# Kernel tuning notes

Measured on AMD Instinct MI355X. Metric: run time of the kernel, lower is better.

Reference implementation:

```python
import jax, jax.numpy as jnp
import numpy as np

L, H, D, E, V, MAXS = 12, 12, 64, 768, 50257, 1024

def _ln(x, g, b, eps=1e-5):
    m = jnp.mean(x, axis=-1, keepdims=True)
    v = jnp.mean(jnp.square(x - m), axis=-1, keepdims=True)
    return (x - m) * jax.lax.rsqrt(v + eps) * g + b

def setup_inputs() -> dict:
    key = jax.random.key(0)
    ks = jax.random.split(key, 16)
    s = 0.02
    inp = {
        "input_ids": jax.random.randint(ks[0], (1, 1), 0, V),
        "past_key": jax.random.normal(ks[1], (L, 1, H, MAXS, D), jnp.float32),
        "past_value": jax.random.normal(ks[2], (L, 1, H, MAXS, D), jnp.float32),
        "past_seq_len": 1023,
        "attention_mask": jnp.ones((1, MAXS), jnp.float32),
        "wte": jax.random.normal(ks[3], (V, E), jnp.float32) * s,
        "wpe": jax.random.normal(ks[4], (MAXS, E), jnp.float32) * s,
        "ln1_g": jnp.ones((L, E), jnp.float32),
        "ln1_b": jnp.zeros((L, E), jnp.float32),
        "attn_w": jax.random.normal(ks[5], (L, E, 3 * E), jnp.float32) * s,
        "attn_b": jnp.zeros((L, 3 * E), jnp.float32),
        "proj_w": jax.random.normal(ks[6], (L, E, E), jnp.float32) * s,
        "proj_b": jnp.zeros((L, E), jnp.float32),
        "ln2_g": jnp.ones((L, E), jnp.float32),
        "ln2_b": jnp.zeros((L, E), jnp.float32),
        "fc_w": jax.random.normal(ks[7], (L, E, 4 * E), jnp.float32) * s,
        "fc_b": jnp.zeros((L, 4 * E), jnp.float32),
        "mlp_w": jax.random.normal(ks[8], (L, 4 * E, E), jnp.float32) * s,
        "mlp_b": jnp.zeros((L, E), jnp.float32),
        "lnf_g": jnp.ones((E,), jnp.float32),
        "lnf_b": jnp.zeros((E,), jnp.float32),
    }
    return inp

def reference(input_ids, past_key, past_value, past_seq_len, attention_mask,
              wte, wpe, ln1_g, ln1_b, attn_w, attn_b, proj_w, proj_b,
              ln2_g, ln2_b, fc_w, fc_b, mlp_w, mlp_b, lnf_g, lnf_b):
    S = int(past_seq_len)  # static cache length
    h = wte[input_ids] + wpe[S]                      # [1,1,E]
    bias = (1.0 - attention_mask[:, :S + 1]) * -1e9  # [1,S+1]
    scale = 1.0 / jnp.sqrt(jnp.float32(D))
    pk, pv = past_key, past_value
    for l in range(L):
        x = _ln(h, ln1_g[l], ln1_b[l])
        qkv = x @ attn_w[l] + attn_b[l]              # [1,1,3E]
        q, k, v = jnp.split(qkv, 3, axis=-1)
        q = q.reshape(1, 1, H, D).transpose(0, 2, 1, 3)  # [1,H,1,D]
        k = k.reshape(1, 1, H, D).transpose(0, 2, 1, 3)
        v = v.reshape(1, 1, H, D).transpose(0, 2, 1, 3)
        k_full = jnp.concatenate([pk[l, :, :, :S, :], k], axis=2)  # [1,H,S+1,D]
        v_full = jnp.concatenate([pv[l, :, :, :S, :], v], axis=2)
        scores = jnp.einsum('bhqd,bhkd->bhqk', q, k_full) * scale
        scores = scores + bias[:, None, None, :]
        attn = jax.nn.softmax(scores, axis=-1)
        o = jnp.einsum('bhqk,bhkd->bhqd', attn, v_full)
        o = o.transpose(0, 2, 1, 3).reshape(1, 1, H * D)
        h = h + o @ proj_w[l] + proj_b[l]
        x2 = _ln(h, ln2_g[l], ln2_b[l])
        h = h + jax.nn.gelu(x2 @ fc_w[l] + fc_b[l], approximate=True) @ mlp_w[l] + mlp_b[l]
        pk = pk.at[l, :, :, S, :].set(k[:, :, 0, :])
        pv = pv.at[l, :, :, S, :].set(v[:, :, 0, :])
    h = _ln(h, lnf_g, lnf_b)
    logits = h @ wte.T                               # [1,1,V] (tied lm_head)
    return (logits, pk, pv)
```

## Files before the change

kernel.cpp:

```cpp
#include <hip/hip_runtime.h>
#include <math.h>

#define EMB 768
#define NH 12
#define HD 64
#define NL 12
#define NV 50257
#define MAXS 1024
#define S_PAST 1023
#define E3 2304
#define E4 3072

#define WS_H    0
#define WS_QKV  768
#define WS_FC   3072
#define WS_PART 6144

__device__ __forceinline__ void blockReduce2(float& a, float& b, volatile float* ra, volatile float* rb) {
  int lane = threadIdx.x & 63, wid = threadIdx.x >> 6;
#pragma unroll
  for (int o = 32; o > 0; o >>= 1) { a += __shfl_down(a, o); b += __shfl_down(b, o); }
  if (lane == 0) { ra[wid] = a; rb[wid] = b; }
  __syncthreads();
  if (threadIdx.x == 0) {
    ra[0] = ra[0] + ra[1] + ra[2] + ra[3];
    rb[0] = rb[0] + rb[1] + rb[2] + rb[3];
  }
  __syncthreads();
  a = ra[0]; b = rb[0];
}

__global__ void init_kernel(const int* __restrict__ ids, const float* __restrict__ wte,
                            const float* __restrict__ wpe, const float* __restrict__ attn_b,
                            float* __restrict__ hvec, float* __restrict__ qkv) {
  int idx = blockIdx.x * 256 + threadIdx.x;
  if (idx < E3) qkv[idx] = attn_b[idx];
  if (idx < EMB) {
    int id = ids[0];
    hvec[idx] = wte[(size_t)id * EMB + idx] + wpe[(size_t)S_PAST * EMB + idx];
  }
}

__global__ void ln_gemv4(const float* __restrict__ hvec, const float* __restrict__ g,
                         const float* __restrict__ bb, const float* __restrict__ W,
                         float* __restrict__ out, int N, int l) {
  __shared__ float lh[EMB];
  __shared__ float xs[32];
  __shared__ float ra[4], rb[4];
  __shared__ float4 red[4][64];
  int tid = threadIdx.x, lane = tid & 63, wid = tid >> 6;
  int e0 = blockIdx.y * 32;
  float hv0 = hvec[tid], hv1 = hvec[tid + 256], hv2 = hvec[tid + 512];
  int j4 = blockIdx.x * 64 + lane;
  int N4 = N >> 2;
  const float4* p = (const float4*)(W + (size_t)l * EMB * N) + (size_t)(e0 + wid) * N4 + j4;
  float4 w[8];
#pragma unroll
  for (int i = 0; i < 8; i++) w[i] = p[(size_t)(i * 4) * N4];
  float gv = 0.f, bv = 0.f;
  if (tid < 32) { gv = g[l * EMB + e0 + tid]; bv = bb[l * EMB + e0 + tid]; }
  lh[tid] = hv0; lh[tid + 256] = hv1; lh[tid + 512] = hv2;
  float s1 = hv0 + hv1 + hv2;
  float s2 = hv0 * hv0 + hv1 * hv1 + hv2 * hv2;
  blockReduce2(s1, s2, ra, rb);
  float mean = s1 * (1.f / EMB);
  float var = s2 * (1.f / EMB) - mean * mean;
  float rstd = rsqrtf(var + 1e-5f);
  if (tid < 32) xs[tid] = (lh[e0 + tid] - mean) * rstd * gv + bv;
  __syncthreads();
  float4 acc = {0.f, 0.f, 0.f, 0.f};
#pragma unroll
  for (int i = 0; i < 8; i++) {
    float x = xs[wid + i * 4];
    acc.x += x * w[i].x; acc.y += x * w[i].y; acc.z += x * w[i].z; acc.w += x * w[i].w;
  }
  red[wid][lane] = acc;
  __syncthreads();
  if (wid == 0) {
    float4 a0 = red[0][lane], a1 = red[1][lane], a2 = red[2][lane], a3 = red[3][lane];
    float rx = a0.x + a1.x + a2.x + a3.x;
    float ry = a0.y + a1.y + a2.y + a3.y;
    float rz = a0.z + a1.z + a2.z + a3.z;
    float rw = a0.w + a1.w + a2.w + a3.w;
    float* op = out + (size_t)j4 * 4;
    atomicAdd(op + 0, rx); atomicAdd(op + 1, ry);
    atomicAdd(op + 2, rz); atomicAdd(op + 3, rw);
  }
}

__global__ void attn_kv(const float* __restrict__ qkv, const float* __restrict__ pk,
                        const float* __restrict__ pv, const float* __restrict__ mask,
                        float* __restrict__ opk, float* __restrict__ opv,
                        float* __restrict__ part, int l) {
  int h = blockIdx.x >> 4, c = blockIdx.x & 15;
  int tid = threadIdx.x, lane = tid & 63, wid = tid >> 6;
  int sub = tid & 15, grp = tid >> 4;
  __shared__ float4 qs4[16];
  __shared__ float sc[64];
  __shared__ float4 redo[4][16];
  if (tid < 16) qs4[tid] = ((const float4*)(qkv + h * 64))[tid];
  __syncthreads();
  size_t base = ((size_t)(l * NH + h) * MAXS) * HD;
  const float4* K4 = (const float4*)(pk + base);
  const float4* V4 = (const float4*)(pv + base);
  float4* oK4 = (float4*)(opk + base);
  float4* oV4 = (float4*)(opv + base);
  int t0 = c * 64;
  float4 kreg[4];
#pragma unroll
  for (int i = 0; i < 4; i++) {
    int t = t0 + grp + i * 16;
    kreg[i] = (t == S_PAST) ? ((const float4*)(qkv + EMB + h * 64))[sub] : K4[(size_t)t * 16 + sub];
  }
#pragma unroll
  for (int i = 0; i < 4; i++) {
    int t = t0 + grp + i * 16;
    oK4[(size_t)t * 16 + sub] = kreg[i];
  }
  float4 q4 = qs4[sub];
#pragma unroll
  for (int i = 0; i < 4; i++) {
    int key = grp + i * 16;
    float p = q4.x * kreg[i].x + q4.y * kreg[i].y + q4.z * kreg[i].z + q4.w * kreg[i].w;
    p += __shfl_xor(p, 1); p += __shfl_xor(p, 2);
    p += __shfl_xor(p, 4); p += __shfl_xor(p, 8);
    if (sub == 0) sc[key] = p * 0.125f + (1.f - mask[t0 + key]) * (-1e9f);
  }
  __syncthreads();
  if (wid == 0) {
    float a = sc[lane];
    float m = a;
#pragma unroll
    for (int o = 32; o > 0; o >>= 1) m = fmaxf(m, __shfl_down(m, o));
    m = __shfl(m, 0);
    float ea = expf(a - m);
    sc[lane] = ea;
    float s = ea;
#pragma unroll
    for (int o = 32; o > 0; o >>= 1) s += __shfl_down(s, o);
    if (lane == 0) { part[(h * 16 + c) * 68 + 0] = m; part[(h * 16 + c) * 68 + 1] = s; }
  }
  __syncthreads();
  float4 vreg[4];
#pragma unroll
  for (int i = 0; i < 4; i++) {
    int t = t0 + grp + i * 16;
    vreg[i] = (t == S_PAST) ? ((const float4*)(qkv + 2 * EMB + h * 64))[sub] : V4[(size_t)t * 16 + sub];
  }
#pragma unroll
  for (int i = 0; i < 4; i++) {
    int t = t0 + grp + i * 16;
    oV4[(size_t)t * 16 + sub] = vreg[i];
  }
  float4 acc = {0.f, 0.f, 0.f, 0.f};
#pragma unroll
  for (int i = 0; i < 4; i++) {
    float w = sc[grp + i * 16];
    acc.x += w * vreg[i].x; acc.y += w * vreg[i].y; acc.z += w * vreg[i].z; acc.w += w * vreg[i].w;
  }
  acc.x += __shfl_xor(acc.x, 16); acc.y += __shfl_xor(acc.y, 16);
  acc.z += __shfl_xor(acc.z, 16); acc.w += __shfl_xor(acc.w, 16);
  acc.x += __shfl_xor(acc.x, 32); acc.y += __shfl_xor(acc.y, 32);
  acc.z += __shfl_xor(acc.z, 32); acc.w += __shfl_xor(acc.w, 32);
  if (lane < 16) redo[wid][lane] = acc;
  __syncthreads();
  if (tid < 16) {
    float4 a0 = redo[0][tid], a1 = redo[1][tid], a2 = redo[2][tid], a3 = redo[3][tid];
    float4 r;
    r.x = a0.x + a1.x + a2.x + a3.x;
    r.y = a0.y + a1.y + a2.y + a3.y;
    r.z = a0.z + a1.z + a2.z + a3.z;
    r.w = a0.w + a1.w + a2.w + a3.w;
    ((float4*)(part + (h * 16 + c) * 68 + 4))[tid] = r;
  }
}

__global__ void proj_attn(const float* __restrict__ part, const float* __restrict__ W,
                          const float* __restrict__ bias, const float* __restrict__ fc_b,
                          float* __restrict__ hout, float* __restrict__ wfc, int l) {
  int jb = blockIdx.x;
  int rt = blockIdx.y;
  int h = rt >> 2, esub = rt & 3;
  int tid = threadIdx.x, lane = tid & 63, wid = tid >> 6;
  __shared__ float xs[16];
  __shared__ float4 red[4][64];
  int j4 = jb * 64 + lane;
  const int N4 = EMB >> 2;
  int r0 = h * 64 + esub * 16;
  const float4* p = (const float4*)(W + (size_t)l * EMB * EMB) + (size_t)(r0 + wid) * N4 + j4;
  float4 w[4];
#pragma unroll
  for (int i = 0; i < 4; i++) w[i] = p[(size_t)(i * 4) * N4];
  if (tid < 16) {
    float M = -1e30f;
#pragma unroll
    for (int q = 0; q < 16; q++) M = fmaxf(M, part[(h * 16 + q) * 68]);
    float T = 0.f, o = 0.f;
    int d = esub * 16 + tid;
#pragma unroll
    for (int q = 0; q < 16; q++) {
      float wq = expf(part[(h * 16 + q) * 68] - M);
      T += part[(h * 16 + q) * 68 + 1] * wq;
      o += part[(h * 16 + q) * 68 + 4 + d] * wq;
    }
    xs[tid] = o / T;
  }
  int bid = rt * 3 + jb;
  if (bid < 12) wfc[bid * 256 + tid] = fc_b[l * E4 + bid * 256 + tid];
  __syncthreads();
  float4 acc = {0.f, 0.f, 0.f, 0.f};
#pragma unroll
  for (int i = 0; i < 4; i++) {
    float x = xs[wid + i * 4];
    acc.x += x * w[i].x; acc.y += x * w[i].y; acc.z += x * w[i].z; acc.w += x * w[i].w;
  }
  red[wid][lane] = acc;
  __syncthreads();
  if (wid == 0) {
    float4 a0 = red[0][lane], a1 = red[1][lane], a2 = red[2][lane], a3 = red[3][lane];
    float rx = a0.x + a1.x + a2.x + a3.x;
    float ry = a0.y + a1.y + a2.y + a3.y;
    float rz = a0.z + a1.z + a2.z + a3.z;
    float rw = a0.w + a1.w + a2.w + a3.w;
    if (rt == 0) {
      const float* bp = bias + l * EMB + jb * 256 + lane * 4;
      rx += bp[0]; ry += bp[1]; rz += bp[2]; rw += bp[3];
    }
    float* op = hout + (size_t)jb * 256 + (size_t)lane * 4;
    atomicAdd(op + 0, rx); atomicAdd(op + 1, ry);
    atomicAdd(op + 2, rz); atomicAdd(op + 3, rw);
  }
}

__global__ void mlp_gemv4(const float* __restrict__ fcv, const float* __restrict__ W,
                          const float* __restrict__ bias, const float* __restrict__ attn_b,
                          float* __restrict__ hout, float* __restrict__ qkv, int l) {
  __shared__ float xs[64];
  __shared__ float4 red[4][64];
  int tid = threadIdx.x, lane = tid & 63, wid = tid >> 6;
  int e0 = blockIdx.y * 64;
  int j4 = blockIdx.x * 64 + lane;
  const int N4 = EMB >> 2;
  const float4* p = (const float4*)(W + (size_t)l * E4 * EMB) + (size_t)(e0 + wid) * N4 + j4;
  float4 w[16];
#pragma unroll
  for (int i = 0; i < 16; i++) w[i] = p[(size_t)(i * 4) * N4];
  if (tid < 64) {
    float x = fcv[e0 + tid];
    xs[tid] = 0.5f * x * (1.f + tanhf(0.7978845608028654f * (x + 0.044715f * x * x * x)));
  }
  int bid = blockIdx.y * 3 + blockIdx.x;
  if (l + 1 < NL && bid < 9) qkv[bid * 256 + tid] = attn_b[(l + 1) * E3 + bid * 256 + tid];
  __syncthreads();
  float4 acc = {0.f, 0.f, 0.f, 0.f};
#pragma unroll
  for (int i = 0; i < 16; i++) {
    float x = xs[wid + i * 4];
    acc.x += x * w[i].x; acc.y += x * w[i].y; acc.z += x * w[i].z; acc.w += x * w[i].w;
  }
  red[wid][lane] = acc;
  __syncthreads();
  if (wid == 0) {
    float4 a0 = red[0][lane], a1 = red[1][lane], a2 = red[2][lane], a3 = red[3][lane];
    float rx = a0.x + a1.x + a2.x + a3.x;
    float ry = a0.y + a1.y + a2.y + a3.y;
    float rz = a0.z + a1.z + a2.z + a3.z;
    float rw = a0.w + a1.w + a2.w + a3.w;
    if (blockIdx.y == 0) {
      const float* bp = bias + l * EMB + j4 * 4;
      rx += bp[0]; ry += bp[1]; rz += bp[2]; rw += bp[3];
    }
    float* op = hout + (size_t)j4 * 4;
    atomicAdd(op + 0, rx); atomicAdd(op + 1, ry);
    atomicAdd(op + 2, rz); atomicAdd(op + 3, rw);
  }
}

__global__ void logits_lnf(const float* __restrict__ hvec, const float* __restrict__ g,
                           const float* __restrict__ b, const float* __restrict__ wte,
                           float* __restrict__ out) {
  __shared__ float4 xs4[192];
  __shared__ float ra[4], rb[4];
  int tid = threadIdx.x, lane = tid & 63, wid = tid >> 6;
  float hv0 = hvec[tid], hv1 = hvec[tid + 256], hv2 = hvec[tid + 512];
  int v = blockIdx.x * 4 + wid;
  float4 a0 = {0,0,0,0}, a1 = {0,0,0,0}, a2 = {0,0,0,0};
  if (v < NV) {
    const float4* row = (const float4*)(wte + (size_t)v * EMB);
    a0 = row[lane]; a1 = row[lane + 64]; a2 = row[lane + 128];
  }
  float s1 = hv0 + hv1 + hv2;
  float s2 = hv0 * hv0 + hv1 * hv1 + hv2 * hv2;
  blockReduce2(s1, s2, ra, rb);
  float mean = s1 * (1.f / EMB);
  float var = s2 * (1.f / EMB) - mean * mean;
  float rstd = rsqrtf(var + 1e-5f);
  ((float*)xs4)[tid]       = (hv0 - mean) * rstd * g[tid]       + b[tid];
  ((float*)xs4)[tid + 256] = (hv1 - mean) * rstd * g[tid + 256] + b[tid + 256];
  ((float*)xs4)[tid + 512] = (hv2 - mean) * rstd * g[tid + 512] + b[tid + 512];
  __syncthreads();
  if (v >= NV) return;
  float4 x0 = xs4[lane], x1 = xs4[lane + 64], x2 = xs4[lane + 128];
  float acc = a0.x * x0.x + a0.y * x0.y + a0.z * x0.z + a0.w * x0.w
            + a1.x * x1.x + a1.y * x1.y + a1.z * x1.z + a1.w * x1.w
            + a2.x * x2.x + a2.y * x2.y + a2.z * x2.z + a2.w * x2.w;
#pragma unroll
  for (int o = 32; o > 0; o >>= 1) acc += __shfl_down(acc, o);
  if (lane == 0) out[v] = acc;
}

extern "C" void kernel_launch(void* const* d_in, const int* in_sizes, int n_in,
                              void* d_out, int out_size, void* d_ws, size_t ws_size,
                              hipStream_t stream) {
  const int* input_ids = (const int*)d_in[0];
  const float* past_key = (const float*)d_in[1];
  const float* past_value = (const float*)d_in[2];
  const float* mask = (const float*)d_in[4];
  const float* wte = (const float*)d_in[5];
  const float* wpe = (const float*)d_in[6];
  const float* ln1_g = (const float*)d_in[7];
  const float* ln1_b = (const float*)d_in[8];
  const float* attn_w = (const float*)d_in[9];
  const float* attn_b = (const float*)d_in[10];
  const float* proj_w = (const float*)d_in[11];
  const float* proj_b = (const float*)d_in[12];
  const float* ln2_g = (const float*)d_in[13];
  const float* ln2_b = (const float*)d_in[14];
  const float* fc_w = (const float*)d_in[15];
  const float* fc_b = (const float*)d_in[16];
  const float* mlp_w = (const float*)d_in[17];
  const float* mlp_b = (const float*)d_in[18];
  const float* lnf_g = (const float*)d_in[19];
  const float* lnf_b = (const float*)d_in[20];

  float* out = (float*)d_out;
  float* out_logits = out;
  float* out_pk = out + NV;
  float* out_pv = out_pk + (size_t)NL * NH * MAXS * HD;

  float* ws = (float*)d_ws;
  float* wh = ws + WS_H;
  float* wqkv = ws + WS_QKV;
  float* wfc = ws + WS_FC;
  float* wpart = ws + WS_PART;

  init_kernel<<<9, 256, 0, stream>>>(input_ids, wte, wpe, attn_b, wh, wqkv);

  for (int l = 0; l < NL; l++) {
    ln_gemv4<<<dim3(9, 24), 256, 0, stream>>>(wh, ln1_g, ln1_b, attn_w, wqkv, E3, l);
    attn_kv<<<192, 256, 0, stream>>>(wqkv, past_key, past_value, mask, out_pk, out_pv, wpart, l);
    proj_attn<<<dim3(3, 48), 256, 0, stream>>>(wpart, proj_w, proj_b, fc_b, wh, wfc, l);
    ln_gemv4<<<dim3(12, 24), 256, 0, stream>>>(wh, ln2_g, ln2_b, fc_w, wfc, E4, l);
    mlp_gemv4<<<dim3(3, 48), 256, 0, stream>>>(wfc, mlp_w, mlp_b, attn_b, wh, wqkv, l);
  }
  logits_lnf<<<12565, 256, 0, stream>>>(wh, lnf_g, lnf_b, wte, out_logits);
}
```

Baseline: 448.5 us.

## Fuse attention output projection into attn kernel and drop proj_attn launch

```diff
diff --git a/kernel.cpp b/kernel.cpp
--- a/kernel.cpp
+++ b/kernel.cpp
@@ -11,10 +11,19 @@
 #define E3 2304
 #define E4 3072
 
-#define WS_H    0
-#define WS_QKV  768
-#define WS_FC   3072
-#define WS_PART 6144
+#define WS_HA   0
+#define WS_HB   768
+#define WS_QKV  1536
+#define WS_FC   3840
+#define WS_Y    6912
+#define WS_T    16128
+
+__device__ __forceinline__ void f4add(float4& a, const float4& b) {
+  a.x += b.x; a.y += b.y; a.z += b.z; a.w += b.w;
+}
+__device__ __forceinline__ void f4fma(float4& a, float x, const float4& w) {
+  a.x += x * w.x; a.y += x * w.y; a.z += x * w.z; a.w += x * w.w;
+}
 
 __device__ __forceinline__ void blockReduce2(float& a, float& b, volatile float* ra, volatile float* rb) {
   int lane = threadIdx.x & 63, wid = threadIdx.x >> 6;
@@ -30,20 +39,27 @@
   a = ra[0]; b = rb[0];
 }
 
+__device__ __forceinline__ float gelu(float x) {
+  return 0.5f * x * (1.f + tanhf(0.7978845608028654f * (x + 0.044715f * x * x * x)));
+}
+
 __global__ void init_kernel(const int* __restrict__ ids, const float* __restrict__ wte,
                             const float* __restrict__ wpe, const float* __restrict__ attn_b,
-                            float* __restrict__ hvec, float* __restrict__ qkv) {
-  int idx = blockIdx.x * 256 + threadIdx.x;
-  if (idx < E3) qkv[idx] = attn_b[idx];
-  if (idx < EMB) {
+                            float* __restrict__ wsf) {
+  int tid = threadIdx.x, bi = blockIdx.x;
+  if (bi < 9) {
+    wsf[WS_QKV + bi * 256 + tid] = attn_b[bi * 256 + tid];
+  } else {
+    int e = (bi - 9) * 256 + tid;
     int id = ids[0];
-    hvec[idx] = wte[(size_t)id * EMB + idx] + wpe[(size_t)S_PAST * EMB + idx];
+    wsf[WS_HA + e] = wte[(size_t)id * EMB + e] + wpe[(size_t)S_PAST * EMB + e];
   }
 }
 
 __global__ void ln_gemv4(const float* __restrict__ hvec, const float* __restrict__ g,
                          const float* __restrict__ bb, const float* __restrict__ W,
-                         float* __restrict__ out, int N, int l) {
+                         float* __restrict__ out, const float* __restrict__ fc_b,
+                         float* __restrict__ wsf, int l) {
   __shared__ float lh[EMB];
   __shared__ float xs[32];
   __shared__ float ra[4], rb[4];
@@ -52,11 +68,18 @@
   int e0 = blockIdx.y * 32;
   float hv0 = hvec[tid], hv1 = hvec[tid + 256], hv2 = hvec[tid + 512];
   int j4 = blockIdx.x * 64 + lane;
-  int N4 = N >> 2;
-  const float4* p = (const float4*)(W + (size_t)l * EMB * N) + (size_t)(e0 + wid) * N4 + j4;
+  const int N4 = E3 >> 2;
+  const float4* p = (const float4*)(W + (size_t)l * EMB * E3) + (size_t)(e0 + wid) * N4 + j4;
   float4 w[8];
 #pragma unroll
   for (int i = 0; i < 8; i++) w[i] = p[(size_t)(i * 4) * N4];
+  if (blockIdx.y == 1) {
+    int t0 = blockIdx.x * 256 + tid;
+    for (int i = t0; i < 9228; i += 2304) wsf[WS_Y + i] = 0.f;
+  } else if (blockIdx.y == 2) {
+    int t0 = blockIdx.x * 256 + tid;
+    for (int i = t0; i < E4; i += 2304) wsf[WS_FC + i] = fc_b[l * E4 + i];
+  }
   float gv = 0.f, bv = 0.f;
   if (tid < 32) { gv = g[l * EMB + e0 + tid]; bv = bb[l * EMB + e0 + tid]; }
   lh[tid] = hv0; lh[tid + 256] = hv1; lh[tid + 512] = hv2;
@@ -70,10 +93,7 @@
   __syncthreads();
   float4 acc = {0.f, 0.f, 0.f, 0.f};
 #pragma unroll
-  for (int i = 0; i < 8; i++) {
-    float x = xs[wid + i * 4];
-    acc.x += x * w[i].x; acc.y += x * w[i].y; acc.z += x * w[i].z; acc.w += x * w[i].w;
-  }
+  for (int i = 0; i < 8; i++) f4fma(acc, xs[wid + i * 4], w[i]);
   red[wid][lane] = acc;
   __syncthreads();
   if (wid == 0) {
@@ -88,15 +108,18 @@
   }
 }
 
-__global__ void attn_kv(const float* __restrict__ qkv, const float* __restrict__ pk,
-                        const float* __restrict__ pv, const float* __restrict__ mask,
-                        float* __restrict__ opk, float* __restrict__ opv,
-                        float* __restrict__ part, int l) {
-  int h = blockIdx.x >> 4, c = blockIdx.x & 15;
+__global__ __launch_bounds__(256) void attn_kv(
+    const float* __restrict__ qkv, const float* __restrict__ pk,
+    const float* __restrict__ pv, const float* __restrict__ mask,
+    const float* __restrict__ proj_w, float* __restrict__ opk, float* __restrict__ opv,
+    float* __restrict__ wsf, int l) {
+  int g = (blockIdx.x & 7) * 24 + (blockIdx.x >> 3);
+  int h = g >> 4, c = g & 15;
   int tid = threadIdx.x, lane = tid & 63, wid = tid >> 6;
   int sub = tid & 15, grp = tid >> 4;
   __shared__ float4 qs4[16];
   __shared__ float sc[64];
+  __shared__ float oc[64];
   __shared__ float4 redo[4][16];
   if (tid < 16) qs4[tid] = ((const float4*)(qkv + h * 64))[tid];
   __syncthreads();
@@ -128,17 +151,12 @@
   }
   __syncthreads();
   if (wid == 0) {
-    float a = sc[lane];
-    float m = a;
-#pragma unroll
-    for (int o = 32; o > 0; o >>= 1) m = fmaxf(m, __shfl_down(m, o));
-    m = __shfl(m, 0);
-    float ea = expf(a - m);
-    sc[lane] = ea;
-    float s = ea;
+    float e = expf(sc[lane]);
+    sc[lane] = e;
+    float s = e;
 #pragma unroll
     for (int o = 32; o > 0; o >>= 1) s += __shfl_down(s, o);
-    if (lane == 0) { part[(h * 16 + c) * 68 + 0] = m; part[(h * 16 + c) * 68 + 1] = s; }
+    if (lane == 0) atomicAdd(wsf + WS_T + h, s);
   }
   __syncthreads();
   float4 vreg[4];
@@ -154,10 +172,7 @@
   }
   float4 acc = {0.f, 0.f, 0.f, 0.f};
 #pragma unroll
-  for (int i = 0; i < 4; i++) {
-    float w = sc[grp + i * 16];
-    acc.x += w * vreg[i].x; acc.y += w * vreg[i].y; acc.z += w * vreg[i].z; acc.w += w * vreg[i].w;
-  }
+  for (int i = 0; i < 4; i++) f4fma(acc, sc[grp + i * 16], vreg[i]);
   acc.x += __shfl_xor(acc.x, 16); acc.y += __shfl_xor(acc.y, 16);
   acc.z += __shfl_xor(acc.z, 16); acc.w += __shfl_xor(acc.w, 16);
   acc.x += __shfl_xor(acc.x, 32); acc.y += __shfl_xor(acc.y, 32);
@@ -171,49 +186,73 @@
     r.y = a0.y + a1.y + a2.y + a3.y;
     r.z = a0.z + a1.z + a2.z + a3.z;
     r.w = a0.w + a1.w + a2.w + a3.w;
-    ((float4*)(part + (h * 16 + c) * 68 + 4))[tid] = r;
-  }
-}
-
-__global__ void proj_attn(const float* __restrict__ part, const float* __restrict__ W,
-                          const float* __restrict__ bias, const float* __restrict__ fc_b,
-                          float* __restrict__ hout, float* __restrict__ wfc, int l) {
-  int jb = blockIdx.x;
-  int rt = blockIdx.y;
-  int h = rt >> 2, esub = rt & 3;
-  int tid = threadIdx.x, lane = tid & 63, wid = tid >> 6;
-  __shared__ float xs[16];
+    ((float4*)oc)[tid] = r;
+  }
+  __syncthreads();
+  if (tid < 192) {
+    const float4* Wp4 = (const float4*)(proj_w + (size_t)l * EMB * EMB)
+                        + (size_t)h * 64 * (EMB >> 2) + tid;
+    float4 pa = {0.f, 0.f, 0.f, 0.f};
+#pragma unroll
+    for (int b = 0; b < 4; b++) {
+      float4 w[16];
+#pragma unroll
+      for (int i = 0; i < 16; i++) w[i] = Wp4[(size_t)(b * 16 + i) * (EMB >> 2)];
+#pragma unroll
+      for (int i = 0; i < 16; i++) f4fma(pa, oc[b * 16 + i], w[i]);
+    }
+    float* yp = wsf + WS_Y + h * EMB + tid * 4;
+    atomicAdd(yp + 0, pa.x); atomicAdd(yp + 1, pa.y);
+    atomicAdd(yp + 2, pa.z); atomicAdd(yp + 3, pa.w);
+  }
+}
+
+__global__ void fc_gemv(const float* __restrict__ R, float* __restrict__ S,
+                        const float* __restrict__ proj_b, const float* __restrict__ g2,
+                        const float* __restrict__ b2, const float* __restrict__ W,
+                        float* __restrict__ wsf, int l) {
+  __shared__ float lh[EMB];
+  __shared__ float xs[32];
+  __shared__ float ra[4], rb[4];
   __shared__ float4 red[4][64];
-  int j4 = jb * 64 + lane;
-  const int N4 = EMB >> 2;
-  int r0 = h * 64 + esub * 16;
-  const float4* p = (const float4*)(W + (size_t)l * EMB * EMB) + (size_t)(r0 + wid) * N4 + j4;
-  float4 w[4];
-#pragma unroll
-  for (int i = 0; i < 4; i++) w[i] = p[(size_t)(i * 4) * N4];
-  if (tid < 16) {
-    float M = -1e30f;
-#pragma unroll
-    for (int q = 0; q < 16; q++) M = fmaxf(M, part[(h * 16 + q) * 68]);
-    float T = 0.f, o = 0.f;
-    int d = esub * 16 + tid;
-#pragma unroll
-    for (int q = 0; q < 16; q++) {
-      float wq = expf(part[(h * 16 + q) * 68] - M);
-      T += part[(h * 16 + q) * 68 + 1] * wq;
-      o += part[(h * 16 + q) * 68 + 4 + d] * wq;
-    }
-    xs[tid] = o / T;
-  }
-  int bid = rt * 3 + jb;
-  if (bid < 12) wfc[bid * 256 + tid] = fc_b[l * E4 + bid * 256 + tid];
+  int tid = threadIdx.x, lane = tid & 63, wid = tid >> 6;
+  int jt = blockIdx.x, et = blockIdx.y, e0 = et * 32;
+  int j4 = jt * 64 + lane;
+  const int N4 = E4 >> 2;
+  const float4* p = (const float4*)(W + (size_t)l * EMB * E4) + (size_t)(e0 + wid) * N4 + j4;
+  float4 w[8];
+#pragma unroll
+  for (int i = 0; i < 8; i++) w[i] = p[(size_t)(i * 4) * N4];
+  float invT[NH];
+#pragma unroll
+  for (int hh = 0; hh < NH; hh++) invT[hh] = 1.f / wsf[WS_T + hh];
+  float hn[3];
+#pragma unroll
+  for (int k = 0; k < 3; k++) {
+    int e = tid + 256 * k;
+    float v = R[e] + proj_b[l * EMB + e];
+#pragma unroll
+    for (int hh = 0; hh < NH; hh++) v += wsf[WS_Y + hh * EMB + e] * invT[hh];
+    hn[k] = v;
+    lh[e] = v;
+  }
+  if (jt == 0 && et == 0) {
+#pragma unroll
+    for (int k = 0; k < 3; k++) S[tid + 256 * k] = hn[k];
+  }
+  float gv = 0.f, bv = 0.f;
+  if (tid < 32) { gv = g2[l * EMB + e0 + tid]; bv = b2[l * EMB + e0 + tid]; }
+  float s1 = hn[0] + hn[1] + hn[2];
+  float s2 = hn[0] * hn[0] + hn[1] * hn[1] + hn[2] * hn[2];
+  blockReduce2(s1, s2, ra, rb);
+  float mean = s1 * (1.f / EMB);
+  float var = s2 * (1.f / EMB) - mean * mean;
+  float rstd = rsqrtf(var + 1e-5f);
+  if (tid < 32) xs[tid] = (lh[e0 + tid] - mean) * rstd * gv + bv;
   __syncthreads();
   float4 acc = {0.f, 0.f, 0.f, 0.f};
 #pragma unroll
-  for (int i = 0; i < 4; i++) {
-    float x = xs[wid + i * 4];
-    acc.x += x * w[i].x; acc.y += x * w[i].y; acc.z += x * w[i].z; acc.w += x * w[i].w;
-  }
+  for (int i = 0; i < 8; i++) f4fma(acc, xs[wid + i * 4], w[i]);
   red[wid][lane] = acc;
   __syncthreads();
   if (wid == 0) {
@@ -222,11 +261,7 @@
     float ry = a0.y + a1.y + a2.y + a3.y;
     float rz = a0.z + a1.z + a2.z + a3.z;
     float rw = a0.w + a1.w + a2.w + a3.w;
-    if (rt == 0) {
-      const float* bp = bias + l * EMB + jb * 256 + lane * 4;
-      rx += bp[0]; ry += bp[1]; rz += bp[2]; rw += bp[3];
-    }
-    float* op = hout + (size_t)jb * 256 + (size_t)lane * 4;
+    float* op = wsf + WS_FC + (size_t)j4 * 4;
     atomicAdd(op + 0, rx); atomicAdd(op + 1, ry);
     atomicAdd(op + 2, rz); atomicAdd(op + 3, rw);
   }
@@ -245,19 +280,13 @@
   float4 w[16];
 #pragma unroll
   for (int i = 0; i < 16; i++) w[i] = p[(size_t)(i * 4) * N4];
-  if (tid < 64) {
-    float x = fcv[e0 + tid];
-    xs[tid] = 0.5f * x * (1.f + tanhf(0.7978845608028654f * (x + 0.044715f * x * x * x)));
-  }
+  if (tid < 64) xs[tid] = gelu(fcv[e0 + tid]);
   int bid = blockIdx.y * 3 + blockIdx.x;
   if (l + 1 < NL && bid < 9) qkv[bid * 256 + tid] = attn_b[(l + 1) * E3 + bid * 256 + tid];
   __syncthreads();
   float4 acc = {0.f, 0.f, 0.f, 0.f};
 #pragma unroll
-  for (int i = 0; i < 16; i++) {
-    float x = xs[wid + i * 4];
-    acc.x += x * w[i].x; acc.y += x * w[i].y; acc.z += x * w[i].z; acc.w += x * w[i].w;
-  }
+  for (int i = 0; i < 16; i++) f4fma(acc, xs[wid + i * 4], w[i]);
   red[wid][lane] = acc;
   __syncthreads();
   if (wid == 0) {
@@ -279,7 +308,7 @@
 __global__ void logits_lnf(const float* __restrict__ hvec, const float* __restrict__ g,
                            const float* __restrict__ b, const float* __restrict__ wte,
                            float* __restrict__ out) {
-  __shared__ float4 xs4[192];
+  __shared__ __align__(16) float4 xs4[192];
   __shared__ float ra[4], rb[4];
   int tid = threadIdx.x, lane = tid & 63, wid = tid >> 6;
   float hv0 = hvec[tid], hv1 = hvec[tid + 256], hv2 = hvec[tid + 512];
@@ -338,20 +367,20 @@
   float* out_pk = out + NV;
   float* out_pv = out_pk + (size_t)NL * NH * MAXS * HD;
 
-  float* ws = (float*)d_ws;
-  float* wh = ws + WS_H;
-  float* wqkv = ws + WS_QKV;
-  float* wfc = ws + WS_FC;
-  float* wpart = ws + WS_PART;
-
-  init_kernel<<<9, 256, 0, stream>>>(input_ids, wte, wpe, attn_b, wh, wqkv);
+  float* wsf = (float*)d_ws;
+  float* wqkv = wsf + WS_QKV;
+  float* wfc = wsf + WS_FC;
+
+  init_kernel<<<12, 256, 0, stream>>>(input_ids, wte, wpe, attn_b, wsf);
 
   for (int l = 0; l < NL; l++) {
-    ln_gemv4<<<dim3(9, 24), 256, 0, stream>>>(wh, ln1_g, ln1_b, attn_w, wqkv, E3, l);
-    attn_kv<<<192, 256, 0, stream>>>(wqkv, past_key, past_value, mask, out_pk, out_pv, wpart, l);
-    proj_attn<<<dim3(3, 48), 256, 0, stream>>>(wpart, proj_w, proj_b, fc_b, wh, wfc, l);
-    ln_gemv4<<<dim3(12, 24), 256, 0, stream>>>(wh, ln2_g, ln2_b, fc_w, wfc, E4, l);
-    mlp_gemv4<<<dim3(3, 48), 256, 0, stream>>>(wfc, mlp_w, mlp_b, attn_b, wh, wqkv, l);
-  }
-  logits_lnf<<<12565, 256, 0, stream>>>(wh, lnf_g, lnf_b, wte, out_logits);
-}
+    float* R = wsf + ((l & 1) ? WS_HB : WS_HA);
+    float* S = wsf + ((l & 1) ? WS_HA : WS_HB);
+    ln_gemv4<<<dim3(9, 24), 256, 0, stream>>>(R, ln1_g, ln1_b, attn_w, wqkv, fc_b, wsf, l);
+    attn_kv<<<192, 256, 0, stream>>>(wqkv, past_key, past_value, mask, proj_w,
+                                     out_pk, out_pv, wsf, l);
+    fc_gemv<<<dim3(12, 24), 256, 0, stream>>>(R, S, proj_b, ln2_g, ln2_b, fc_w, wsf, l);
+    mlp_gemv4<<<dim3(3, 48), 256, 0, stream>>>(wfc, mlp_w, mlp_b, attn_b, S, wqkv, l);
+  }
+  logits_lnf<<<12565, 256, 0, stream>>>(wsf + WS_HA, lnf_g, lnf_b, wte, out_logits);
+}
```

New measurement: 458.8 us. +2.3%, slower.
